# Kernel optimization log

Measured on AMD Instinct MI355X. Metric: run time of the kernel, lower is better.

The kernel has to match this reference:

```python
import jax, jax.numpy as jnp
import numpy as np

B, S, D = 32, 512, 512      # batch, seq_len, d_model
H, K = 16, 32               # head_num, head_dim
A = 256                     # attention_hidden_dim


def setup_inputs() -> dict:
    key = jax.random.key(0)
    ks = jax.random.split(key, 10)
    s = lambda fan_in: 1.0 / np.sqrt(fan_in)
    return {
        "x":   jax.random.normal(ks[0], (B, S, D), dtype=jnp.float32),
        # per-head Q projections: Linear(D, D), stored [H, in, out]
        "Qw":  jax.random.normal(ks[1], (H, D, D), dtype=jnp.float32) * s(D),
        "Qb":  jax.random.normal(ks[2], (H, D), dtype=jnp.float32) * s(D),
        # per-head V projections: Linear(D, K)
        "Vw":  jax.random.normal(ks[3], (H, D, K), dtype=jnp.float32) * s(D),
        "Vb":  jax.random.normal(ks[4], (H, K), dtype=jnp.float32) * s(D),
        # additive attention pooling: Linear(H*K, A) then Linear(A, 1)
        "Wv":  jax.random.normal(ks[5], (H * K, A), dtype=jnp.float32) * s(H * K),
        "bv":  jax.random.normal(ks[6], (A,), dtype=jnp.float32) * s(H * K),
        "wq":  jax.random.normal(ks[7], (A, 1), dtype=jnp.float32) * s(A),
        "bq":  jax.random.normal(ks[8], (1,), dtype=jnp.float32) * s(A),
    }


def reference(x, Qw, Qb, Vw, Vb, Wv, bv, wq, bq):
    # per-head query projection: [B, H, S, D]
    q = jnp.einsum("bsd,hde->bhse", x, Qw) + Qb[None, :, None, :]
    # raw scores: [B, H, S, S] (s = query pos, t = key pos)
    scores = jnp.einsum("bhse,bte->bhst", q, x)
    # NOTE: softmax over dim=-2 (the QUERY axis), not the usual key axis
    attn = jax.nn.softmax(scores, axis=-2)
    # context: [B, H, S, D]
    ctx = jnp.einsum("bhst,btd->bhsd", attn, x)
    # per-head value projection then concat heads -> [B, S, H*K]
    head_out = jnp.einsum("bhsd,hdk->bshk", ctx, Vw) + Vb[None, None, :, :]
    h = head_out.reshape(B, S, H * K)
    # dropout is identity at inference
    # additive attention pooling
    a = jnp.tanh(h @ Wv + bv) @ wq + bq          # [B, S, 1]
    z = jnp.einsum("bs,bsk->bk", a[..., 0], h)   # [B, H*K]
    return z
```

## Files before the change

### kernel.cpp

```cpp
#include <hip/hip_runtime.h>

#define DEVFN __device__ __forceinline__

typedef _Float16 f16;
typedef _Float16 f16x8 __attribute__((ext_vector_type(8)));
typedef _Float16 f16x4 __attribute__((ext_vector_type(4)));
typedef _Float16 f16x2 __attribute__((ext_vector_type(2)));
typedef float    f32x4 __attribute__((ext_vector_type(4)));

enum { NB = 32, NS = 512, ND = 512, NH = 16, NK = 32, NA = 256 };

#define SZ(x) ((size_t)(x))

typedef __attribute__((address_space(3))) void       as3_void;
typedef const __attribute__((address_space(1))) void as1_cvoid;
DEVFN void ldsdma16(const void* g, void* l) {
  __builtin_amdgcn_global_load_lds((as1_cvoid*)g, (as3_void*)l, 16, 0, 0);
}

DEVFN int xcd_swz(int flat, int n) {
  return (flat & 7) * (n >> 3) + (flat >> 3);
}

DEVFN void gemm256_pipe(const f16* __restrict__ Ag, const f16* __restrict__ Bg,
                        int lda, int ldb, f16* smem, f32x4 acc[8][4]) {
  const int tid  = threadIdx.x;
  const int lane = tid & 63;
  const int wid  = tid >> 6;
  const int wr   = wid >> 2;
  const int wcn  = wid & 3;
  const int s_r  = tid >> 3;
  const int s_g  = tid & 7;
  const int frow = lane & 15;
  const int fg   = lane >> 4;

  auto stageA = [&](int t, int h) {
    f16* base = smem + (t & 1) * 32768;
    const f16* G = Ag + t * 64;
#pragma unroll
    for (int j = 0; j < 2; ++j) {
      int row = j * 128 + h * 64 + s_r;
      ldsdma16(G + SZ(row) * lda + ((s_g ^ (row & 7)) * 8), base + row * 64 + s_g * 8);
    }
  };
  auto stageB = [&](int t, int h) {
    f16* base = smem + (t & 1) * 32768 + 16384;
    const f16* G = Bg + t * 64;
#pragma unroll
    for (int j = 0; j < 2; ++j) {
      int row = (j * 2 + (s_r >> 5)) * 64 + h * 32 + (s_r & 31);
      ldsdma16(G + SZ(row) * ldb + ((s_g ^ (row & 7)) * 8), base + row * 64 + s_g * 8);
    }
  };
  auto rdA = [&](int t, int row, int kk) -> f16x8 {
    const f16* base = smem + (t & 1) * 32768;
    return *(const f16x8*)(base + row * 64 + (((kk * 4 + fg) ^ (row & 7)) * 8));
  };
  auto rdB = [&](int t, int row, int kk) -> f16x8 {
    const f16* base = smem + (t & 1) * 32768 + 16384;
    return *(const f16x8*)(base + row * 64 + (((kk * 4 + fg) ^ (row & 7)) * 8));
  };

  f16x8 af[8], bf0[4], bf1[4];

#define QUAD(a, b, BF)                                                          \
  _Pragma("unroll")                                                             \
  for (int mi = 0; mi < 4; ++mi)                                                \
    _Pragma("unroll")                                                           \
    for (int ni = 0; ni < 2; ++ni)                                              \
      _Pragma("unroll")                                                         \
      for (int kk = 0; kk < 2; ++kk)                                            \
        acc[(a)*4 + mi][(b)*2 + ni] = __builtin_amdgcn_mfma_f32_16x16x32_f16(   \
            af[mi * 2 + kk], BF[ni * 2 + kk], acc[(a)*4 + mi][(b)*2 + ni], 0, 0, 0);

#define PHASE_TAIL(MFMA_BLOCK)                              \
  __builtin_amdgcn_s_barrier();                             \
  asm volatile("s_waitcnt lgkmcnt(0)" ::: "memory");        \
  __builtin_amdgcn_sched_barrier(0);                        \
  __builtin_amdgcn_s_setprio(1);                            \
  MFMA_BLOCK                                                \
  __builtin_amdgcn_s_setprio(0);                            \
  __builtin_amdgcn_sched_barrier(0);

  stageA(0, 0); stageB(0, 0); stageB(0, 1); stageA(0, 1);
  stageA(1, 0); stageB(1, 0); stageB(1, 1);
  asm volatile("s_waitcnt vmcnt(6)" ::: "memory");
  __builtin_amdgcn_s_barrier();

  for (int t = 0; t < 8; ++t) {
#pragma unroll
    for (int mi = 0; mi < 4; ++mi)
#pragma unroll
      for (int kk = 0; kk < 2; ++kk)
        af[mi * 2 + kk] = rdA(t, wr * 128 + mi * 16 + frow, kk);
#pragma unroll
    for (int ni = 0; ni < 2; ++ni)
#pragma unroll
      for (int kk = 0; kk < 2; ++kk)
        bf0[ni * 2 + kk] = rdB(t, wcn * 64 + ni * 16 + frow, kk);
    if (t <= 6) stageA(t + 1, 1);
    PHASE_TAIL(QUAD(0, 0, bf0))
    __builtin_amdgcn_s_barrier();

#pragma unroll
    for (int ni = 0; ni < 2; ++ni)
#pragma unroll
      for (int kk = 0; kk < 2; ++kk)
        bf1[ni * 2 + kk] = rdB(t, wcn * 64 + 32 + ni * 16 + frow, kk);
    if (t <= 5) stageA(t + 2, 0);
    PHASE_TAIL(QUAD(0, 1, bf1))
    __builtin_amdgcn_s_barrier();

#pragma unroll
    for (int mi = 0; mi < 4; ++mi)
#pragma unroll
      for (int kk = 0; kk < 2; ++kk)
        af[mi * 2 + kk] = rdA(t, wr * 128 + 64 + mi * 16 + frow, kk);
    if (t <= 5) stageB(t + 2, 0);
    PHASE_TAIL(QUAD(1, 1, bf1))
    __builtin_amdgcn_s_barrier();

    if (t <= 5) stageB(t + 2, 1);
    PHASE_TAIL(QUAD(1, 0, bf0))
    if (t < 6)       asm volatile("s_waitcnt vmcnt(6)" ::: "memory");
    else if (t == 6) asm volatile("s_waitcnt vmcnt(0)" ::: "memory");
    __builtin_amdgcn_s_barrier();
  }
#undef QUAD
#undef PHASE_TAIL
}

DEVFN void gemm_core_128(const f16* __restrict__ Ag, const f16* __restrict__ Bg,
                         int lda, int ldb, int nk, f16* lds, f32x4 acc[4][4]) {
  f16* As = lds;
  f16* Bs = lds + 128 * 64;
  const int tid  = threadIdx.x;
  const int lane = tid & 63;
  const int wvid = tid >> 6, wr = wvid >> 1, wc = wvid & 1;
  const int srow = tid >> 3, scol = (tid & 7) * 8;
  const int frow = lane & 15, fk = (lane >> 4) * 8;
  for (int ks = 0; ks < nk; ++ks) {
    const f16* ga = Ag + ks * 64 + scol;
    const f16* gb = Bg + ks * 64 + scol;
#pragma unroll
    for (int r = 0; r < 4; ++r) {
      ldsdma16(ga + SZ(r * 32 + srow) * lda, As + SZ(r * 32 + srow) * 64 + scol);
      ldsdma16(gb + SZ(r * 32 + srow) * ldb, Bs + SZ(r * 32 + srow) * 64 + scol);
    }
    __syncthreads();
#pragma unroll
    for (int kk = 0; kk < 64; kk += 32) {
      f16x8 a[4], b[4];
#pragma unroll
      for (int i = 0; i < 4; ++i)
        a[i] = *(const f16x8*)(As + SZ(wr * 64 + i * 16 + frow) * 64 + kk + fk);
#pragma unroll
      for (int j = 0; j < 4; ++j)
        b[j] = *(const f16x8*)(Bs + SZ(wc * 64 + j * 16 + frow) * 64 + kk + fk);
#pragma unroll
      for (int i = 0; i < 4; ++i)
#pragma unroll
        for (int j = 0; j < 4; ++j)
          acc[i][j] = __builtin_amdgcn_mfma_f32_16x16x32_f16(a[i], b[j], acc[i][j], 0, 0, 0);
    }
    __syncthreads();
  }
}

DEVFN void wlds_write(f16* wlds, int row, int col, f16 v) {
  int byte = (row * 256 + col * 2) ^ ((row & 7) << 4);
  *(f16*)((char*)wlds + byte) = v;
}
DEVFN f16x8 wlds_read8(const f16* wlds, int row, int col) {
  int byte = (row * 256 + col * 2) ^ ((row & 7) << 4);
  return *(const f16x8*)((const char*)wlds + byte);
}

__global__ __launch_bounds__(256) void k_cast4(const float* __restrict__ s,
                                               f16* __restrict__ d, int n4) {
  int i = blockIdx.x * 256 + threadIdx.x;
  if (i >= n4) return;
  float4 v = ((const float4*)s)[i];
  f16x4 o; o[0] = (f16)v.x; o[1] = (f16)v.y; o[2] = (f16)v.z; o[3] = (f16)v.w;
  ((f16x4*)d)[i] = o;
}

__global__ void k_tcast(const float* __restrict__ src, f16* __restrict__ dst,
                        int R, int C, long sStride, long dStride) {
  __shared__ float tile[32][33];
  src += (long)blockIdx.z * sStride;
  dst += (long)blockIdx.z * dStride;
  int c0 = blockIdx.x * 32, r0 = blockIdx.y * 32;
  int tx = threadIdx.x, ty = threadIdx.y;
#pragma unroll
  for (int i = 0; i < 4; ++i)
    tile[ty + 8 * i][tx] = src[(long)(r0 + ty + 8 * i) * C + c0 + tx];
  __syncthreads();
#pragma unroll
  for (int i = 0; i < 4; ++i)
    dst[(long)(c0 + ty + 8 * i) * R + r0 + tx] = (f16)tile[tx][ty + 8 * i];
}

__global__ __launch_bounds__(256) void k_gemm_xv(const f16* __restrict__ xh,
                                                 const f16* __restrict__ vwt,
                                                 f16* __restrict__ xvt) {
  __shared__ f16 smem[128 * 64 * 2];
  int z = blockIdx.z, b = z >> 2, hg = z & 3, tm = blockIdx.x;
  f32x4 acc[4][4] = {};
  gemm_core_128(xh + SZ(b) * NS * ND + SZ(tm) * 128 * ND,
                vwt + SZ(hg) * 4 * NK * ND, ND, ND, ND / 64, smem, acc);
  int tid = threadIdx.x, lane = tid & 63, wvid = tid >> 6, wr = wvid >> 1, wc = wvid & 1;
  int rbase = (lane >> 4) * 4, cbase = lane & 15;
#pragma unroll
  for (int mi = 0; mi < 4; ++mi)
#pragma unroll
    for (int ni = 0; ni < 4; ++ni) {
      int n = wc * 64 + ni * 16 + cbase;
      int hh = hg * 4 + (n >> 5), kk = n & 31;
#pragma unroll
      for (int r = 0; r < 4; ++r) {
        int t = tm * 128 + wr * 64 + mi * 16 + rbase + r;
        xvt[(SZ(b * NH + hh) * NK + kk) * NS + t] = (f16)acc[mi][ni][r];
      }
    }
}

__global__ __launch_bounds__(512, 2) void k_gemm_q256(const f16* __restrict__ xh,
                                                      const f16* __restrict__ qwt,
                                                      const float* __restrict__ Qb,
                                                      f16* __restrict__ qc, int b0) {
  __shared__ f16 smem[65536];
  int n = gridDim.x;
  int lg = xcd_swz(blockIdx.x, n);
  int tm2 = lg & 1, tn2 = (lg >> 1) & 1, bhl = lg >> 2;
  int b = b0 + (bhl >> 4), h = bhl & 15;
  f32x4 acc[8][4] = {};
  gemm256_pipe(xh + SZ(b) * NS * ND + SZ(tm2) * 256 * ND,
               qwt + SZ(h) * ND * ND + SZ(tn2) * 256 * ND, ND, ND, smem, acc);
  int lane = threadIdx.x & 63, wid = threadIdx.x >> 6;
  int wr = wid >> 2, wcn = wid & 3;
  int rbase = (lane >> 4) * 4, cbase = lane & 15;
  f16* qb = qc + SZ(bhl) * NS * ND;
#pragma unroll
  for (int mi = 0; mi < 8; ++mi)
#pragma unroll
    for (int ni = 0; ni < 4; ++ni) {
      int colg = tn2 * 256 + wcn * 64 + ni * 16 + cbase;
      float bias = Qb[h * ND + colg];
#pragma unroll
      for (int r = 0; r < 4; ++r) {
        int rowg = tm2 * 256 + wr * 128 + mi * 16 + rbase + r;
        qb[SZ(rowg) * ND + colg] = (f16)(acc[mi][ni][r] + bias);
      }
    }
}

__global__ __launch_bounds__(512, 2) void k_scores256(const f16* __restrict__ qc,
                                                      const f16* __restrict__ xh,
                                                      f16* __restrict__ sc,
                                                      float* __restrict__ mp,
                                                      float* __restrict__ zp, int b0) {
  __shared__ f16 smem[65536];
  int n = gridDim.x;
  int lg = xcd_swz(blockIdx.x, n);
  int st2 = lg & 1, tt2 = (lg >> 1) & 1, bhl = lg >> 2;
  int b = b0 + (bhl >> 4);
  f32x4 acc[8][4] = {};
  gemm256_pipe(qc + SZ(bhl) * NS * ND + SZ(st2) * 256 * ND,
               xh + SZ(b) * NS * ND + SZ(tt2) * 256 * ND, ND, ND, smem, acc);
  int tid = threadIdx.x, lane = tid & 63, wid = tid >> 6;
  int wr = wid >> 2, wcn = wid & 3;
  __syncthreads();
  float* sbuf = (float*)smem;

  float mh[4];
#pragma unroll
  for (int ni = 0; ni < 4; ++ni) {
    float m = -1e30f;
#pragma unroll
    for (int mi = 0; mi < 8; ++mi)
#pragma unroll
      for (int r = 0; r < 4; ++r) m = fmaxf(m, acc[mi][ni][r]);
    m = fmaxf(m, __shfl_xor(m, 16));
    m = fmaxf(m, __shfl_xor(m, 32));
    mh[ni] = m;
  }
  if (lane < 16) {
#pragma unroll
    for (int ni = 0; ni < 4; ++ni)
      sbuf[wr * 256 + wcn * 64 + ni * 16 + lane] = mh[ni];
  }
  __syncthreads();
  int cb_ = lane & 15;
  float tmc[4];
#pragma unroll
  for (int ni = 0; ni < 4; ++ni) {
    int col = wcn * 64 + ni * 16 + cb_;
    tmc[ni] = fmaxf(sbuf[col], sbuf[256 + col]);
  }
  f16x4* scb = (f16x4*)(sc + SZ(lg) * 65536);
  float sm[4] = {0.f, 0.f, 0.f, 0.f};
#pragma unroll
  for (int mi = 0; mi < 8; ++mi)
#pragma unroll
    for (int ni = 0; ni < 4; ++ni) {
      f16x4 o;
#pragma unroll
      for (int r = 0; r < 4; ++r) {
        float ev = __expf(acc[mi][ni][r] - tmc[ni]);
        o[r] = (f16)ev;
        sm[ni] += ev;
      }
      scb[((wid * 8 + mi) * 4 + ni) * 64 + lane] = o;
    }
#pragma unroll
  for (int ni = 0; ni < 4; ++ni) {
    sm[ni] += __shfl_xor(sm[ni], 16);
    sm[ni] += __shfl_xor(sm[ni], 32);
  }
  if (lane < 16) {
#pragma unroll
    for (int ni = 0; ni < 4; ++ni)
      sbuf[512 + wr * 256 + wcn * 64 + ni * 16 + lane] = sm[ni];
  }
  __syncthreads();
  if (tid < 256) {
    float m  = fmaxf(sbuf[tid], sbuf[256 + tid]);
    float zz = sbuf[512 + tid] + sbuf[768 + tid];
    size_t idx = (SZ(bhl) * 2 + st2) * NS + tt2 * 256 + tid;
    mp[idx] = m; zp[idx] = zz;
  }
}

__global__ __launch_bounds__(256) void k_stats_combine(const float* __restrict__ mp,
                                                       const float* __restrict__ zp,
                                                       float* __restrict__ cs) {
  int i = blockIdx.x * 256 + threadIdx.x;
  int bhl = i >> 9, t = i & (NS - 1);
  float m0 = mp[(SZ(bhl) * 2 + 0) * NS + t];
  float m1 = mp[(SZ(bhl) * 2 + 1) * NS + t];
  float m = fmaxf(m0, m1);
  float e0 = __expf(m0 - m), e1 = __expf(m1 - m);
  float Z = zp[(SZ(bhl) * 2 + 0) * NS + t] * e0 + zp[(SZ(bhl) * 2 + 1) * NS + t] * e1;
  float rZ = 1.0f / Z;
  cs[(SZ(bhl) * 2 + 0) * NS + t] = e0 * rZ;
  cs[(SZ(bhl) * 2 + 1) * NS + t] = e1 * rZ;
}

__global__ __launch_bounds__(256) void k_norm_pv(const f16* __restrict__ sc,
                                                 const f16* __restrict__ xvt,
                                                 const float* __restrict__ cs,
                                                 const float* __restrict__ Vb,
                                                 f16* __restrict__ h16, int b0) {
  __shared__ f16 wlds[128 * 128];
  int bhl = blockIdx.y, b = b0 + (bhl >> 4), h = bhl & 15;
  int st = blockIdx.x;
  int tid = threadIdx.x, lane = tid & 63, wvid = tid >> 6, wr = wvid >> 1, wc = wvid & 1;
  int rbase = (lane >> 4) * 4, cbase = lane & 15, fk = (lane >> 4) * 8;
  f32x4 acc2[2][2] = {};
  const f16* xvh = xvt + SZ(b * NH + h) * NK * NS;
  for (int tt = 0; tt < 4; ++tt) {
    int blk = (bhl * 2 + (tt >> 1)) * 2 + (st >> 1);
    const f16x4* scb = (const f16x4*)(sc + SZ(blk) * 65536);
    int wave_sc = (st & 1) * 4 + ((tt & 1) * 2 + wc);
#pragma unroll
    for (int ni = 0; ni < 4; ++ni) {
      int tl = wc * 64 + ni * 16 + cbase;
      float csv = cs[(SZ(bhl) * 2 + (st >> 1)) * NS + tt * 128 + tl];
#pragma unroll
      for (int mi = 0; mi < 4; ++mi) {
        int mi_sc = wr * 4 + mi;
        f16x4 v = scb[((wave_sc * 8 + mi_sc) * 4 + ni) * 64 + lane];
#pragma unroll
        for (int r = 0; r < 4; ++r) {
          int sl = wr * 64 + mi * 16 + rbase + r;
          wlds_write(wlds, sl, tl, (f16)((float)v[r] * csv));
        }
      }
    }
    __syncthreads();
    const f16* xvb = xvh + tt * 128;
#pragma unroll
    for (int tc = 0; tc < 4; ++tc) {
      f16x8 aw[2], bx[2];
#pragma unroll
      for (int m2 = 0; m2 < 2; ++m2)
        aw[m2] = wlds_read8(wlds, wvid * 32 + m2 * 16 + cbase, tc * 32 + fk);
#pragma unroll
      for (int n2 = 0; n2 < 2; ++n2)
        bx[n2] = *(const f16x8*)(xvb + SZ(n2 * 16 + cbase) * NS + tc * 32 + fk);
#pragma unroll
      for (int m2 = 0; m2 < 2; ++m2)
#pragma unroll
        for (int n2 = 0; n2 < 2; ++n2)
          acc2[m2][n2] = __builtin_amdgcn_mfma_f32_16x16x32_f16(aw[m2], bx[n2], acc2[m2][n2], 0, 0, 0);
    }
    __syncthreads();
  }
  const float* vb = Vb + h * NK;
#pragma unroll
  for (int m2 = 0; m2 < 2; ++m2)
#pragma unroll
    for (int n2 = 0; n2 < 2; ++n2)
#pragma unroll
      for (int r = 0; r < 4; ++r) {
        int sg = st * 128 + wvid * 32 + m2 * 16 + rbase + r;
        int kk = n2 * 16 + cbase;
        float val = acc2[m2][n2][r] + vb[kk];
        h16[SZ(b * NS + sg) * (NH * NK) + h * NK + kk] = (f16)val;
      }
}

__global__ __launch_bounds__(256) void k_gemm_u(const f16* __restrict__ h16,
                                                const f16* __restrict__ wvt,
                                                const float* __restrict__ bv,
                                                f16* __restrict__ U) {
  __shared__ f16 smem[128 * 64 * 2];
  int tm = blockIdx.x, tn = blockIdx.y;
  f32x4 acc[4][4] = {};
  gemm_core_128(h16 + SZ(tm) * 128 * ND, wvt + SZ(tn) * 128 * ND, ND, ND, ND / 64, smem, acc);
  int tid = threadIdx.x, lane = tid & 63, wvid = tid >> 6, wr = wvid >> 1, wc = wvid & 1;
  int rbase = (lane >> 4) * 4, cbase = lane & 15;
#pragma unroll
  for (int mi = 0; mi < 4; ++mi)
#pragma unroll
    for (int ni = 0; ni < 4; ++ni) {
      int colg = tn * 128 + wc * 64 + ni * 16 + cbase;
      float bias = bv[colg];
#pragma unroll
      for (int r = 0; r < 4; ++r) {
        int rowg = tm * 128 + wr * 64 + mi * 16 + rbase + r;
        U[SZ(rowg) * NA + colg] = (f16)tanhf(acc[mi][ni][r] + bias);
      }
    }
}

__global__ __launch_bounds__(256) void k_a(const f16* __restrict__ U,
                                           const float* __restrict__ wq,
                                           const float* __restrict__ bq,
                                           float* __restrict__ a) {
  int wid = (blockIdx.x * 256 + threadIdx.x) >> 6;
  int lane = threadIdx.x & 63;
  const f16* u = U + SZ(wid) * NA;
  float p = 0.f;
#pragma unroll
  for (int j = 0; j < NA / 64; ++j) p += (float)u[lane + 64 * j] * wq[lane + 64 * j];
#pragma unroll
  for (int o = 32; o; o >>= 1) p += __shfl_xor(p, o);
  if (lane == 0) a[wid] = p + bq[0];
}

__global__ __launch_bounds__(256) void k_zpart(const f16* __restrict__ h16,
                                               const float* __restrict__ a,
                                               float* __restrict__ zpt) {
  int b = blockIdx.y, c = blockIdx.x, tid = threadIdx.x;
  float z0 = 0.f, z1 = 0.f;
  for (int s = 0; s < 64; ++s) {
    int sg = c * 64 + s;
    float av = a[b * NS + sg];
    const f16* hr = h16 + SZ(b * NS + sg) * (NH * NK);
    f16x2 v = ((const f16x2*)hr)[tid];
    z0 += av * (float)v[0];
    z1 += av * (float)v[1];
  }
  zpt[SZ(b * 8 + c) * 512 + 2 * tid]     = z0;
  zpt[SZ(b * 8 + c) * 512 + 2 * tid + 1] = z1;
}

__global__ __launch_bounds__(256) void k_zred(const float* __restrict__ zpt,
                                              float* __restrict__ out) {
  int i = blockIdx.x * 256 + threadIdx.x;
  int b = i >> 9, k = i & 511;
  float z = 0.f;
#pragma unroll
  for (int c = 0; c < 8; ++c) z += zpt[SZ(b * 8 + c) * 512 + k];
  out[i] = z;
}

static size_t ws_plan(int cb, size_t off[14]) {
  size_t o = 0;
  auto put = [&](size_t bytes) { size_t r = o; o += (bytes + 255) & ~SZ(255); return r; };
  off[0]  = put(SZ(NB) * NS * ND * 2);
  off[1]  = put(SZ(NH) * ND * ND * 2);
  off[2]  = put(SZ(NA) * ND * 2);
  off[3]  = put(SZ(NH) * NK * ND * 2);
  off[4]  = put(SZ(NB) * NH * NK * NS * 2);
  off[5]  = put(SZ(cb) * NH * NS * ND * 2);
  off[6]  = put(SZ(cb) * NH * NS * NS * 2);
  off[7]  = put(SZ(cb) * NH * 2 * NS * 4);
  off[8]  = put(SZ(cb) * NH * 2 * NS * 4);
  off[9]  = put(SZ(cb) * NH * 2 * NS * 4);
  off[10] = put(SZ(NB) * NS * NH * NK * 2);
  off[11] = put(SZ(NB) * NS * NA * 2);
  off[12] = put(SZ(NB) * NS * 4);
  off[13] = put(SZ(NB) * 8 * NH * NK * 4);
  return o;
}

extern "C" void kernel_launch(void* const* d_in, const int* in_sizes, int n_in,
                              void* d_out, int out_size, void* d_ws, size_t ws_size,
                              hipStream_t stream) {
  const float* x  = (const float*)d_in[0];
  const float* Qw = (const float*)d_in[1];
  const float* Qb = (const float*)d_in[2];
  const float* Vw = (const float*)d_in[3];
  const float* Vb = (const float*)d_in[4];
  const float* Wv = (const float*)d_in[5];
  const float* bv = (const float*)d_in[6];
  const float* wq = (const float*)d_in[7];
  const float* bq = (const float*)d_in[8];

  int cbv = 0;
  size_t off[14];
  const int cand[5] = {32, 16, 8, 4, 2};
  for (int ci = 0; ci < 5; ++ci) {
    if (ws_plan(cand[ci], off) <= ws_size) { cbv = cand[ci]; break; }
  }
  if (cbv == 0) return;

  char* ws = (char*)d_ws;
  f16*   xh   = (f16*)(ws + off[0]);
  f16*   qwt  = (f16*)(ws + off[1]);
  f16*   wvt  = (f16*)(ws + off[2]);
  f16*   vwt  = (f16*)(ws + off[3]);
  f16*   xvt  = (f16*)(ws + off[4]);
  f16*   qc   = (f16*)(ws + off[5]);
  f16*   sc   = (f16*)(ws + off[6]);
  float* mp   = (float*)(ws + off[7]);
  float* zps  = (float*)(ws + off[8]);
  float* cs   = (float*)(ws + off[9]);
  f16*   h16  = (f16*)(ws + off[10]);
  f16*   U    = (f16*)(ws + off[11]);
  float* a    = (float*)(ws + off[12]);
  float* zpt  = (float*)(ws + off[13]);
  float* zout = (float*)d_out;

  k_cast4<<<SZ(NB) * NS * ND / 4 / 256, 256, 0, stream>>>(x, xh, NB * NS * ND / 4);
  k_tcast<<<dim3(16, 16, 16), dim3(32, 8), 0, stream>>>(Qw, qwt, ND, ND, (long)ND * ND, (long)ND * ND);
  k_tcast<<<dim3(8, 16, 1), dim3(32, 8), 0, stream>>>(Wv, wvt, ND, NA, 0, 0);
  k_tcast<<<dim3(1, 16, 16), dim3(32, 8), 0, stream>>>(Vw, vwt, ND, NK, (long)ND * NK, (long)NK * ND);
  k_gemm_xv<<<dim3(4, 1, NB * 4), 256, 0, stream>>>(xh, vwt, xvt);

  for (int b0 = 0; b0 < NB; b0 += cbv) {
    k_gemm_q256<<<cbv * 64, 512, 0, stream>>>(xh, qwt, Qb, qc, b0);
    k_scores256<<<cbv * 64, 512, 0, stream>>>(qc, xh, sc, mp, zps, b0);
    k_stats_combine<<<cbv * NH * NS / 256, 256, 0, stream>>>(mp, zps, cs);
    k_norm_pv<<<dim3(4, cbv * NH), 256, 0, stream>>>(sc, xvt, cs, Vb, h16, b0);
  }

  k_gemm_u<<<dim3(NB * NS / 128, 2, 1), 256, 0, stream>>>(h16, wvt, bv, U);
  k_a<<<NB * NS / 4, 256, 0, stream>>>(U, wq, bq, a);
  k_zpart<<<dim3(8, NB), 256, 0, stream>>>(h16, a, zpt);
  k_zred<<<NB * 512 / 256, 256, 0, stream>>>(zpt, zout);
}
```

Before: 509.2 us.

## Make each 256-tile GEMM block compute two N-tiles with a continuous pipeline

The Q-projection and score GEMMs now have each workgroup loop over both 256-column halves in one 16-step software pipeline. A per-half epilogue runs mid-loop, and accumulators are reset between halves. This halves the grid, amortises the pipeline prologue and drain, and lets loads for the second half overlap the first half's tail. It also drops the explicit lgkmcnt wait and sched_barrier around MFMA phases and adds a separate LDS buffer for softmax stats. The trade-offs are fewer blocks, which lowers occupancy and parallelism, and the epilogue now stalls the pipeline mid-loop while stage loads are in flight.

Result: slower. 966.3 us (+89.8%).

```diff
diff --git a/kernel.cpp b/kernel.cpp
--- a/kernel.cpp
+++ b/kernel.cpp
@@ -22,8 +22,9 @@
   return (flat & 7) * (n >> 3) + (flat >> 3);
 }
 
-DEVFN void gemm256_pipe(const f16* __restrict__ Ag, const f16* __restrict__ Bg,
-                        int lda, int ldb, f16* smem, f32x4 acc[8][4]) {
+template <class EPI>
+DEVFN void gemm256x2(const f16* __restrict__ Ag, const f16* __restrict__ Bg,
+                     int lda, int ldb, f16* smem, EPI epi) {
   const int tid  = threadIdx.x;
   const int lane = tid & 63;
   const int wid  = tid >> 6;
@@ -34,30 +35,32 @@
   const int frow = lane & 15;
   const int fg   = lane >> 4;
 
-  auto stageA = [&](int t, int h) {
-    f16* base = smem + (t & 1) * 32768;
-    const f16* G = Ag + t * 64;
+  f32x4 acc[8][4] = {};
+
+  auto stageA = [&](int vt, int h) {
+    f16* base = smem + (vt & 1) * 32768;
+    const f16* G = Ag + (vt & 7) * 64;
 #pragma unroll
     for (int j = 0; j < 2; ++j) {
       int row = j * 128 + h * 64 + s_r;
       ldsdma16(G + SZ(row) * lda + ((s_g ^ (row & 7)) * 8), base + row * 64 + s_g * 8);
     }
   };
-  auto stageB = [&](int t, int h) {
-    f16* base = smem + (t & 1) * 32768 + 16384;
-    const f16* G = Bg + t * 64;
+  auto stageB = [&](int vt, int h) {
+    f16* base = smem + (vt & 1) * 32768 + 16384;
+    const f16* G = Bg + SZ(vt >> 3) * 256 * ldb + (vt & 7) * 64;
 #pragma unroll
     for (int j = 0; j < 2; ++j) {
       int row = (j * 2 + (s_r >> 5)) * 64 + h * 32 + (s_r & 31);
       ldsdma16(G + SZ(row) * ldb + ((s_g ^ (row & 7)) * 8), base + row * 64 + s_g * 8);
     }
   };
-  auto rdA = [&](int t, int row, int kk) -> f16x8 {
-    const f16* base = smem + (t & 1) * 32768;
+  auto rdA = [&](int vt, int row, int kk) -> f16x8 {
+    const f16* base = smem + (vt & 1) * 32768;
     return *(const f16x8*)(base + row * 64 + (((kk * 4 + fg) ^ (row & 7)) * 8));
   };
-  auto rdB = [&](int t, int row, int kk) -> f16x8 {
-    const f16* base = smem + (t & 1) * 32768 + 16384;
+  auto rdB = [&](int vt, int row, int kk) -> f16x8 {
+    const f16* base = smem + (vt & 1) * 32768 + 16384;
     return *(const f16x8*)(base + row * 64 + (((kk * 4 + fg) ^ (row & 7)) * 8));
   };
 
@@ -73,61 +76,67 @@
         acc[(a)*4 + mi][(b)*2 + ni] = __builtin_amdgcn_mfma_f32_16x16x32_f16(   \
             af[mi * 2 + kk], BF[ni * 2 + kk], acc[(a)*4 + mi][(b)*2 + ni], 0, 0, 0);
 
-#define PHASE_TAIL(MFMA_BLOCK)                              \
-  __builtin_amdgcn_s_barrier();                             \
-  asm volatile("s_waitcnt lgkmcnt(0)" ::: "memory");        \
-  __builtin_amdgcn_sched_barrier(0);                        \
-  __builtin_amdgcn_s_setprio(1);                            \
-  MFMA_BLOCK                                                \
-  __builtin_amdgcn_s_setprio(0);                            \
-  __builtin_amdgcn_sched_barrier(0);
+#define MFMA_PHASE(MB)                   \
+  __builtin_amdgcn_s_barrier();          \
+  __builtin_amdgcn_s_setprio(1);         \
+  MB                                     \
+  __builtin_amdgcn_s_setprio(0);
 
   stageA(0, 0); stageB(0, 0); stageB(0, 1); stageA(0, 1);
   stageA(1, 0); stageB(1, 0); stageB(1, 1);
   asm volatile("s_waitcnt vmcnt(6)" ::: "memory");
   __builtin_amdgcn_s_barrier();
 
-  for (int t = 0; t < 8; ++t) {
+  for (int vt = 0; vt < 16; ++vt) {
 #pragma unroll
     for (int mi = 0; mi < 4; ++mi)
 #pragma unroll
       for (int kk = 0; kk < 2; ++kk)
-        af[mi * 2 + kk] = rdA(t, wr * 128 + mi * 16 + frow, kk);
+        af[mi * 2 + kk] = rdA(vt, wr * 128 + mi * 16 + frow, kk);
 #pragma unroll
     for (int ni = 0; ni < 2; ++ni)
 #pragma unroll
       for (int kk = 0; kk < 2; ++kk)
-        bf0[ni * 2 + kk] = rdB(t, wcn * 64 + ni * 16 + frow, kk);
-    if (t <= 6) stageA(t + 1, 1);
-    PHASE_TAIL(QUAD(0, 0, bf0))
+        bf0[ni * 2 + kk] = rdB(vt, wcn * 64 + ni * 16 + frow, kk);
+    if (vt <= 14) stageA(vt + 1, 1);
+    MFMA_PHASE(QUAD(0, 0, bf0))
     __builtin_amdgcn_s_barrier();
 
 #pragma unroll
     for (int ni = 0; ni < 2; ++ni)
 #pragma unroll
       for (int kk = 0; kk < 2; ++kk)
-        bf1[ni * 2 + kk] = rdB(t, wcn * 64 + 32 + ni * 16 + frow, kk);
-    if (t <= 5) stageA(t + 2, 0);
-    PHASE_TAIL(QUAD(0, 1, bf1))
+        bf1[ni * 2 + kk] = rdB(vt, wcn * 64 + 32 + ni * 16 + frow, kk);
+    if (vt <= 13) stageA(vt + 2, 0);
+    MFMA_PHASE(QUAD(0, 1, bf1))
     __builtin_amdgcn_s_barrier();
 
 #pragma unroll
     for (int mi = 0; mi < 4; ++mi)
 #pragma unroll
       for (int kk = 0; kk < 2; ++kk)
-        af[mi * 2 + kk] = rdA(t, wr * 128 + 64 + mi * 16 + frow, kk);
-    if (t <= 5) stageB(t + 2, 0);
-    PHASE_TAIL(QUAD(1, 1, bf1))
+        af[mi * 2 + kk] = rdA(vt, wr * 128 + 64 + mi * 16 + frow, kk);
+    if (vt <= 13) stageB(vt + 2, 0);
+    MFMA_PHASE(QUAD(1, 1, bf1))
     __builtin_amdgcn_s_barrier();
 
-    if (t <= 5) stageB(t + 2, 1);
-    PHASE_TAIL(QUAD(1, 0, bf0))
-    if (t < 6)       asm volatile("s_waitcnt vmcnt(6)" ::: "memory");
-    else if (t == 6) asm volatile("s_waitcnt vmcnt(0)" ::: "memory");
+    if (vt <= 13) stageB(vt + 2, 1);
+    MFMA_PHASE(QUAD(1, 0, bf0))
+    if (vt <= 13)      asm volatile("s_waitcnt vmcnt(6)" ::: "memory");
+    else if (vt == 14) asm volatile("s_waitcnt vmcnt(0)" ::: "memory");
     __builtin_amdgcn_s_barrier();
+
+    if (vt == 7) {
+      epi(0, acc);
+#pragma unroll
+      for (int mi = 0; mi < 8; ++mi)
+#pragma unroll
+        for (int ni = 0; ni < 4; ++ni) acc[mi][ni] = f32x4{0.f, 0.f, 0.f, 0.f};
+    }
   }
+  epi(1, acc);
 #undef QUAD
-#undef PHASE_TAIL
+#undef MFMA_PHASE
 }
 
 DEVFN void gemm_core_128(const f16* __restrict__ Ag, const f16* __restrict__ Bg,
@@ -232,27 +241,28 @@
   __shared__ f16 smem[65536];
   int n = gridDim.x;
   int lg = xcd_swz(blockIdx.x, n);
-  int tm2 = lg & 1, tn2 = (lg >> 1) & 1, bhl = lg >> 2;
+  int tm2 = lg & 1, bhl = lg >> 1;
   int b = b0 + (bhl >> 4), h = bhl & 15;
-  f32x4 acc[8][4] = {};
-  gemm256_pipe(xh + SZ(b) * NS * ND + SZ(tm2) * 256 * ND,
-               qwt + SZ(h) * ND * ND + SZ(tn2) * 256 * ND, ND, ND, smem, acc);
   int lane = threadIdx.x & 63, wid = threadIdx.x >> 6;
   int wr = wid >> 2, wcn = wid & 3;
   int rbase = (lane >> 4) * 4, cbase = lane & 15;
   f16* qb = qc + SZ(bhl) * NS * ND;
-#pragma unroll
-  for (int mi = 0; mi < 8; ++mi)
-#pragma unroll
-    for (int ni = 0; ni < 4; ++ni) {
-      int colg = tn2 * 256 + wcn * 64 + ni * 16 + cbase;
-      float bias = Qb[h * ND + colg];
-#pragma unroll
-      for (int r = 0; r < 4; ++r) {
-        int rowg = tm2 * 256 + wr * 128 + mi * 16 + rbase + r;
-        qb[SZ(rowg) * ND + colg] = (f16)(acc[mi][ni][r] + bias);
+  auto epi = [&](int hB, f32x4 (&acc)[8][4]) {
+#pragma unroll
+    for (int mi = 0; mi < 8; ++mi)
+#pragma unroll
+      for (int ni = 0; ni < 4; ++ni) {
+        int colg = hB * 256 + wcn * 64 + ni * 16 + cbase;
+        float bias = Qb[h * ND + colg];
+#pragma unroll
+        for (int r = 0; r < 4; ++r) {
+          int rowg = tm2 * 256 + wr * 128 + mi * 16 + rbase + r;
+          qb[SZ(rowg) * ND + colg] = (f16)(acc[mi][ni][r] + bias);
+        }
       }
-    }
+  };
+  gemm256x2(xh + SZ(b) * NS * ND + SZ(tm2) * 256 * ND,
+            qwt + SZ(h) * ND * ND, ND, ND, smem, epi);
 }
 
 __global__ __launch_bounds__(512, 2) void k_scores256(const f16* __restrict__ qc,
@@ -261,75 +271,76 @@
                                                       float* __restrict__ mp,
                                                       float* __restrict__ zp, int b0) {
   __shared__ f16 smem[65536];
+  __shared__ float sbuf[1024];
   int n = gridDim.x;
   int lg = xcd_swz(blockIdx.x, n);
-  int st2 = lg & 1, tt2 = (lg >> 1) & 1, bhl = lg >> 2;
+  int st2 = lg & 1, bhl = lg >> 1;
   int b = b0 + (bhl >> 4);
-  f32x4 acc[8][4] = {};
-  gemm256_pipe(qc + SZ(bhl) * NS * ND + SZ(st2) * 256 * ND,
-               xh + SZ(b) * NS * ND + SZ(tt2) * 256 * ND, ND, ND, smem, acc);
   int tid = threadIdx.x, lane = tid & 63, wid = tid >> 6;
   int wr = wid >> 2, wcn = wid & 3;
-  __syncthreads();
-  float* sbuf = (float*)smem;
-
-  float mh[4];
-#pragma unroll
-  for (int ni = 0; ni < 4; ++ni) {
-    float m = -1e30f;
+  auto epi = [&](int hB, f32x4 (&acc)[8][4]) {
+    __syncthreads();
+    float mh[4];
+#pragma unroll
+    for (int ni = 0; ni < 4; ++ni) {
+      float m = -1e30f;
+#pragma unroll
+      for (int mi = 0; mi < 8; ++mi)
+#pragma unroll
+        for (int r = 0; r < 4; ++r) m = fmaxf(m, acc[mi][ni][r]);
+      m = fmaxf(m, __shfl_xor(m, 16));
+      m = fmaxf(m, __shfl_xor(m, 32));
+      mh[ni] = m;
+    }
+    if (lane < 16) {
+#pragma unroll
+      for (int ni = 0; ni < 4; ++ni)
+        sbuf[wr * 256 + wcn * 64 + ni * 16 + lane] = mh[ni];
+    }
+    __syncthreads();
+    int cb_ = lane & 15;
+    float tmc[4];
+#pragma unroll
+    for (int ni = 0; ni < 4; ++ni) {
+      int col = wcn * 64 + ni * 16 + cb_;
+      tmc[ni] = fmaxf(sbuf[col], sbuf[256 + col]);
+    }
+    int lgE = bhl * 4 + hB * 2 + st2;
+    f16x4* scb = (f16x4*)(sc + SZ(lgE) * 65536);
+    float sm[4] = {0.f, 0.f, 0.f, 0.f};
 #pragma unroll
     for (int mi = 0; mi < 8; ++mi)
 #pragma unroll
-      for (int r = 0; r < 4; ++r) m = fmaxf(m, acc[mi][ni][r]);
-    m = fmaxf(m, __shfl_xor(m, 16));
-    m = fmaxf(m, __shfl_xor(m, 32));
-    mh[ni] = m;
-  }
-  if (lane < 16) {
-#pragma unroll
-    for (int ni = 0; ni < 4; ++ni)
-      sbuf[wr * 256 + wcn * 64 + ni * 16 + lane] = mh[ni];
-  }
-  __syncthreads();
-  int cb_ = lane & 15;
-  float tmc[4];
-#pragma unroll
-  for (int ni = 0; ni < 4; ++ni) {
-    int col = wcn * 64 + ni * 16 + cb_;
-    tmc[ni] = fmaxf(sbuf[col], sbuf[256 + col]);
-  }
-  f16x4* scb = (f16x4*)(sc + SZ(lg) * 65536);
-  float sm[4] = {0.f, 0.f, 0.f, 0.f};
-#pragma unroll
-  for (int mi = 0; mi < 8; ++mi)
+      for (int ni = 0; ni < 4; ++ni) {
+        f16x4 o;
+#pragma unroll
+        for (int r = 0; r < 4; ++r) {
+          float ev = __expf(acc[mi][ni][r] - tmc[ni]);
+          o[r] = (f16)ev;
+          sm[ni] += ev;
+        }
+        scb[((wid * 8 + mi) * 4 + ni) * 64 + lane] = o;
+      }
 #pragma unroll
     for (int ni = 0; ni < 4; ++ni) {
-      f16x4 o;
-#pragma unroll
-      for (int r = 0; r < 4; ++r) {
-        float ev = __expf(acc[mi][ni][r] - tmc[ni]);
-        o[r] = (f16)ev;
-        sm[ni] += ev;
-      }
-      scb[((wid * 8 + mi) * 4 + ni) * 64 + lane] = o;
-    }
-#pragma unroll
-  for (int ni = 0; ni < 4; ++ni) {
-    sm[ni] += __shfl_xor(sm[ni], 16);
-    sm[ni] += __shfl_xor(sm[ni], 32);
-  }
-  if (lane < 16) {
-#pragma unroll
-    for (int ni = 0; ni < 4; ++ni)
-      sbuf[512 + wr * 256 + wcn * 64 + ni * 16 + lane] = sm[ni];
-  }
-  __syncthreads();
-  if (tid < 256) {
-    float m  = fmaxf(sbuf[tid], sbuf[256 + tid]);
-    float zz = sbuf[512 + tid] + sbuf[768 + tid];
-    size_t idx = (SZ(bhl) * 2 + st2) * NS + tt2 * 256 + tid;
-    mp[idx] = m; zp[idx] = zz;
-  }
+      sm[ni] += __shfl_xor(sm[ni], 16);
+      sm[ni] += __shfl_xor(sm[ni], 32);
+    }
+    if (lane < 16) {
+#pragma unroll
+      for (int ni = 0; ni < 4; ++ni)
+        sbuf[512 + wr * 256 + wcn * 64 + ni * 16 + lane] = sm[ni];
+    }
+    __syncthreads();
+    if (tid < 256) {
+      float m  = fmaxf(sbuf[tid], sbuf[256 + tid]);
+      float zz = sbuf[512 + tid] + sbuf[768 + tid];
+      size_t idx = (SZ(bhl) * 2 + st2) * NS + hB * 256 + tid;
+      mp[idx] = m; zp[idx] = zz;
+    }
+  };
+  gemm256x2(qc + SZ(bhl) * NS * ND + SZ(st2) * 256 * ND,
+            xh + SZ(b) * NS * ND, ND, ND, smem, epi);
 }
 
 __global__ __launch_bounds__(256) void k_stats_combine(const float* __restrict__ mp,
@@ -542,8 +553,8 @@
   k_gemm_xv<<<dim3(4, 1, NB * 4), 256, 0, stream>>>(xh, vwt, xvt);
 
   for (int b0 = 0; b0 < NB; b0 += cbv) {
-    k_gemm_q256<<<cbv * 64, 512, 0, stream>>>(xh, qwt, Qb, qc, b0);
-    k_scores256<<<cbv * 64, 512, 0, stream>>>(qc, xh, sc, mp, zps, b0);
+    k_gemm_q256<<<cbv * 32, 512, 0, stream>>>(xh, qwt, Qb, qc, b0);
+    k_scores256<<<cbv * 32, 512, 0, stream>>>(qc, xh, sc, mp, zps, b0);
     k_stats_combine<<<cbv * NH * NS / 256, 256, 0, stream>>>(mp, zps, cs);
     k_norm_pv<<<dim3(4, cbv * NH), 256, 0, stream>>>(sc, xvt, cs, Vb, h16, b0);
   }
```
